# Optimization experiments

Measured on AMD Instinct MI355X. Metric: run time of the kernel, lower is better.

Reference implementation:

```python
import jax, jax.numpy as jnp
import numpy as np

TAU = 2.0
BN_EPS = 1e-5
SG_ALPHA = 4.0
ATTN_SCALE = 0.125
NUM_HEADS = 8
T, B, C, H, W = 2, 16, 256, 64, 64


@jax.custom_vjp
def heaviside(x):
    return (x >= 0.0).astype(x.dtype)

def _hv_fwd(x):
    return (x >= 0.0).astype(x.dtype), x

def _hv_bwd(x, g):
    s = jax.nn.sigmoid(SG_ALPHA * x)
    return (g * SG_ALPHA * s * (1.0 - s),)

heaviside.defvjp(_hv_fwd, _hv_bwd)


def lif(x_seq, v_th):
    # MultiStepLIFNode: v <- v + (x - v)/tau ; spike = H(v - v_th); hard reset to 0 (detached)
    def step(v, x):
        v = v + (x - v) / TAU
        s = heaviside(v - v_th)
        v = v * (1.0 - jax.lax.stop_gradient(s))
        return v, s
    _, spikes = jax.lax.scan(step, jnp.zeros_like(x_seq[0]), x_seq)
    return spikes


def bn1d(x, gamma, beta, mean, var):
    # eval-mode BatchNorm1d over channel axis 2 of [T,B,C,N]
    inv = (gamma / jnp.sqrt(var + BN_EPS)).reshape(1, 1, -1, 1)
    shift = (beta - mean * gamma / jnp.sqrt(var + BN_EPS)).reshape(1, 1, -1, 1)
    return x * inv + shift


def to_heads(t):
    # [T,B,C,N] -> [T,B,h,N,d]
    t_, b_, c_, n_ = t.shape
    d = c_ // NUM_HEADS
    return t.transpose(0, 1, 3, 2).reshape(t_, b_, n_, NUM_HEADS, d).transpose(0, 1, 3, 2, 4)


def setup_inputs() -> dict:
    key = jax.random.key(0)
    ks = jax.random.split(key, 24)
    w_scale = 0.06  # ~1/sqrt(C)
    inp = {
        'x': jax.random.normal(ks[0], (T, B, C, H, W), jnp.float32),
        'wq': jax.random.normal(ks[1], (C, C), jnp.float32) * w_scale,
        'wk': jax.random.normal(ks[2], (C, C), jnp.float32) * w_scale,
        'wv': jax.random.normal(ks[3], (C, C), jnp.float32) * w_scale,
        'wp': jax.random.normal(ks[4], (C, C), jnp.float32) * w_scale,
        'bp': jax.random.normal(ks[5], (C,), jnp.float32) * 0.1,
    }
    i = 6
    for p in ('q', 'k', 'v', 'p'):
        inp[p + '_gamma'] = jax.random.uniform(ks[i], (C,), jnp.float32, 0.5, 1.5); i += 1
        inp[p + '_beta'] = jax.random.normal(ks[i], (C,), jnp.float32) * 0.1; i += 1
        inp[p + '_mean'] = jax.random.normal(ks[i], (C,), jnp.float32) * 0.1; i += 1
        inp[p + '_var'] = jax.random.uniform(ks[i], (C,), jnp.float32, 0.5, 1.5); i += 1
    return inp


def reference(x, wq, wk, wv, wp, bp,
              q_gamma, q_beta, q_mean, q_var,
              k_gamma, k_beta, k_mean, k_var,
              v_gamma, v_beta, v_mean, v_var,
              p_gamma, p_beta, p_mean, p_var):
    t_, b_, c_, h_, w_ = x.shape
    n_ = h_ * w_
    xs = lif(x, 1.0).reshape(t_, b_, c_, n_)  # proj_lif then flatten(3)
    # 1x1 conv == channel matmul, then BN, then LIF (binary spikes)
    q_out = lif(bn1d(jnp.einsum('oc,tbcn->tbon', wq, xs), q_gamma, q_beta, q_mean, q_var), 1.0)
    k_out = lif(bn1d(jnp.einsum('oc,tbcn->tbon', wk, xs), k_gamma, k_beta, k_mean, k_var), 1.0)
    v_out = lif(bn1d(jnp.einsum('oc,tbcn->tbon', wv, xs), v_gamma, v_beta, v_mean, v_var), 1.0)
    q = to_heads(q_out)
    k = to_heads(k_out)
    v = to_heads(v_out)
    # linear attention: (k^T @ v) then q @ (k^T v)
    kv = jnp.einsum('tbhnd,tbhne->tbhde', k, v)  # [T,B,h,d,d]
    attn = jnp.einsum('tbhnd,tbhde->tbhne', q, kv) * ATTN_SCALE
    attn = attn.transpose(0, 1, 2, 4, 3).reshape(t_, b_, c_, n_)
    s = lif(attn, 0.5)  # attn_lif with v_threshold=0.5
    out = jnp.einsum('oc,tbcn->tbon', wp, s) + bp.reshape(1, 1, -1, 1)
    out = bn1d(out, p_gamma, p_beta, p_mean, p_var).reshape(t_, b_, c_, h_, w_)
    return (out, xs, q_out, k_out, v_out)
```

## Files before the change

kernel.cpp:

```cpp
#include <hip/hip_runtime.h>
#include <cstdint>
#include <cstddef>

typedef __attribute__((ext_vector_type(8))) short short8;
typedef __attribute__((ext_vector_type(4))) float floatx4;
typedef __attribute__((ext_vector_type(4))) unsigned int uintx4;
typedef __attribute__((ext_vector_type(4))) unsigned short ushort4x;

#define DEV static __device__ __forceinline__

constexpr int NT = 2, NB = 16, NC = 256, NN = 4096, NHD = 8;
constexpr size_t NE1 = (size_t)NT * NB * NC * NN;
constexpr size_t TSTRIDE = (size_t)NB * NC * NN;

DEV unsigned short f2bf(float x) {
  unsigned int u = __builtin_bit_cast(unsigned int, x);
  unsigned int lsb = (u >> 16) & 1u;
  u += 0x7FFFu + lsb;
  return (unsigned short)(u >> 16);
}
DEV float bfb2f(unsigned short h) {
  unsigned int u = ((unsigned int)h) << 16;
  return __builtin_bit_cast(float, u);
}
DEV unsigned short spike2bf(float s) {
  return (unsigned short)(__builtin_bit_cast(unsigned int, s) >> 16);
}
DEV unsigned int pk2(unsigned short a, unsigned short b) {
  return (unsigned int)a | ((unsigned int)b << 16);
}
typedef __attribute__((address_space(3))) unsigned int lds_u32;
typedef __attribute__((address_space(1))) const unsigned int glb_u32;
DEV void gld_lds16(const void* g, void* l) {
  __builtin_amdgcn_global_load_lds((glb_u32*)g, (lds_u32*)l, 16, 0, 0);
}

__global__ __launch_bounds__(256) void prep_kernel(
    const float* __restrict__ wq, const float* __restrict__ wk, const float* __restrict__ wv,
    const float* __restrict__ wp, const float* __restrict__ bp,
    const float* __restrict__ qg, const float* __restrict__ qb, const float* __restrict__ qm, const float* __restrict__ qva,
    const float* __restrict__ kg, const float* __restrict__ kb, const float* __restrict__ km, const float* __restrict__ kva,
    const float* __restrict__ vg, const float* __restrict__ vb, const float* __restrict__ vm, const float* __restrict__ vva,
    const float* __restrict__ pg, const float* __restrict__ pb, const float* __restrict__ pm, const float* __restrict__ pva,
    unsigned short* __restrict__ Wqkv, unsigned short* __restrict__ Wp,
    float* __restrict__ invqkv, float* __restrict__ shqkv,
    float* __restrict__ invp, float* __restrict__ shp)
{
  int idx = blockIdx.x * 256 + threadIdx.x;
  if (idx < 196608) {
    int o = idx >> 8, c = idx & 255;
    const float* src = (o < 256) ? wq : (o < 512) ? wk : wv;
    float w = src[(size_t)(o & 255) * 256 + c];
    unsigned short h0 = f2bf(w);  float f0 = bfb2f(h0);
    float r1 = w - f0;
    unsigned short h1 = f2bf(r1); float f1 = bfb2f(h1);
    float r2 = r1 - f1;
    unsigned short h2 = f2bf(r2);
    Wqkv[idx] = h0; Wqkv[196608 + idx] = h1; Wqkv[393216 + idx] = h2;
  } else if (idx < 262144) {
    int j = idx - 196608;
    float w = wp[j];
    unsigned short h0 = f2bf(w);  float f0 = bfb2f(h0);
    float r1 = w - f0;
    unsigned short h1 = f2bf(r1); float f1 = bfb2f(h1);
    float r2 = r1 - f1;
    unsigned short h2 = f2bf(r2);
    Wp[j] = h0; Wp[65536 + j] = h1; Wp[131072 + j] = h2;
  } else if (idx < 262912) {
    int i = idx - 262144;
    int p = i >> 8, c = i & 255;
    float g  = (p == 0) ? qg[c] : (p == 1) ? kg[c] : vg[c];
    float be = (p == 0) ? qb[c] : (p == 1) ? kb[c] : vb[c];
    float mn = (p == 0) ? qm[c] : (p == 1) ? km[c] : vm[c];
    float vr = (p == 0) ? qva[c] : (p == 1) ? kva[c] : vva[c];
    float sq = sqrtf(vr + 1e-5f);
    invqkv[i] = g / sq;
    shqkv[i]  = be - (mn * g) / sq;
  } else if (idx < 263168) {
    int c = idx - 262912;
    float sq = sqrtf(pva[c] + 1e-5f);
    float iv = pg[c] / sq;
    invp[c] = iv;
    shp[c]  = pb[c] - (pm[c] * pg[c]) / sq + bp[c] * iv;
  }
}

__global__ __launch_bounds__(256) void lifx_kernel(const float* __restrict__ x,
                                                   float* __restrict__ xs_out,
                                                   unsigned short* __restrict__ xs_t)
{
  __shared__ float tile[2][64][65];
  const int nt = blockIdx.x, ct = blockIdx.y, b = blockIdx.z;
  const int tid = threadIdx.x;
  const int ci = tid >> 2, cq = tid & 3;
  const int n0 = nt * 64, c0 = ct * 64;
  const size_t rowbase = ((size_t)(b * NC + c0 + ci)) * NN + n0 + cq * 16;
  const float* px0 = x + rowbase;
  const float* px1 = x + rowbase + TSTRIDE;
  float* po0 = xs_out + rowbase;
  float* po1 = xs_out + rowbase + TSTRIDE;
  #pragma unroll
  for (int jj = 0; jj < 4; jj++) {
    floatx4 x0 = *(const floatx4*)(px0 + jj * 4);
    floatx4 x1 = *(const floatx4*)(px1 + jj * 4);
    floatx4 s0v, s1v;
    #pragma unroll
    for (int e = 0; e < 4; e++) {
      float v1 = x0[e] * 0.5f;
      float s0 = (v1 >= 1.0f) ? 1.0f : 0.0f;
      float vr = v1 * (1.0f - s0);
      float v2 = vr + (x1[e] - vr) * 0.5f;
      float s1 = (v2 >= 1.0f) ? 1.0f : 0.0f;
      s0v[e] = s0; s1v[e] = s1;
      tile[0][ci][cq * 16 + jj * 4 + e] = s0;
      tile[1][ci][cq * 16 + jj * 4 + e] = s1;
    }
    *(floatx4*)(po0 + jj * 4) = s0v;
    *(floatx4*)(po1 + jj * 4) = s1v;
  }
  __syncthreads();
  const int ni = tid >> 2, cg = tid & 3;
  #pragma unroll
  for (int t = 0; t < 2; t++) {
    unsigned short* dst = xs_t + ((size_t)((t * NB + b) * NN) + n0 + ni) * NC + c0 + cg * 16;
    uintx4 w0, w1;
    #pragma unroll
    for (int p2 = 0; p2 < 4; p2++) {
      w0[p2] = pk2(spike2bf(tile[t][cg * 16 + p2 * 2    ][ni]),
                   spike2bf(tile[t][cg * 16 + p2 * 2 + 1][ni]));
      w1[p2] = pk2(spike2bf(tile[t][cg * 16 + p2 * 2 + 8][ni]),
                   spike2bf(tile[t][cg * 16 + p2 * 2 + 9][ni]));
    }
    *(uintx4*)dst = w0;
    *(uintx4*)(dst + 8) = w1;
  }
}

__global__ __launch_bounds__(256, 3) void qkv_gemm(
    const unsigned short* __restrict__ xs_t,
    const unsigned short* __restrict__ Wsp,
    const float* __restrict__ invv, const float* __restrict__ shv,
    float* __restrict__ dq, float* __restrict__ dk, float* __restrict__ dv)
{
  __shared__ __align__(16) unsigned char smem[33280];
  unsigned short* Al = (unsigned short*)smem;
  unsigned short* Bl = (unsigned short*)(smem + 24576);
  float* yl = (float*)smem;
  const int nt = blockIdx.x, mt = blockIdx.y, b = blockIdx.z;
  const int tid = threadIdx.x;
  const int lane = tid & 63, quad = lane >> 4, l16 = lane & 15;
  const int wave = tid >> 6;
  const int tw = wave >> 1, wm = (wave & 1) * 64;
  floatx4 acc[4][4] = {};

  for (int k0 = 0; k0 < 256; k0 += 32) {
    __syncthreads();
    #pragma unroll
    for (int j = 0; j < 6; j++) {
      int ci = j * 256 + tid;
      int s = ci >> 9, j2 = ci & 511, row = j2 >> 2, kk = j2 & 3;
      const unsigned short* g = Wsp + (size_t)s * 196608 + (size_t)(mt * 128 + row) * 256 + k0 + kk * 8;
      gld_lds16(g, Al + ci * 8);
    }
    #pragma unroll
    for (int j = 0; j < 2; j++) {
      int ci = j * 256 + tid;
      int t = ci >> 8, j2 = ci & 255, row = j2 >> 2, kk = j2 & 3;
      const unsigned short* g = xs_t + ((size_t)((t * NB + b) * NN) + nt * 64 + row) * NC + k0 + kk * 8;
      gld_lds16(g, Bl + ci * 8);
    }
    __syncthreads();

    short8 bfr[4];
    #pragma unroll
    for (int ni = 0; ni < 4; ni++)
      bfr[ni] = *(const short8*)(Bl + ((size_t)(tw * 64 + ni * 16 + l16)) * 32 + quad * 8);
    #pragma unroll
    for (int mi = 0; mi < 4; mi++) {
      const int arow = wm + mi * 16 + l16;
      short8 a0 = *(const short8*)(Al + ((size_t)(          arow)) * 32 + quad * 8);
      short8 a1 = *(const short8*)(Al + ((size_t)(128  +   arow)) * 32 + quad * 8);
      short8 a2 = *(const short8*)(Al + ((size_t)(256  +   arow)) * 32 + quad * 8);
      #pragma unroll
      for (int ni = 0; ni < 4; ni++) {
        acc[mi][ni] = __builtin_amdgcn_mfma_f32_16x16x32_bf16(a0, bfr[ni], acc[mi][ni], 0, 0, 0);
        acc[mi][ni] = __builtin_amdgcn_mfma_f32_16x16x32_bf16(a1, bfr[ni], acc[mi][ni], 0, 0, 0);
        acc[mi][ni] = __builtin_amdgcn_mfma_f32_16x16x32_bf16(a2, bfr[ni], acc[mi][ni], 0, 0, 0);
      }
    }
  }
  __syncthreads();
  if (tw == 0) {
    #pragma unroll
    for (int mi = 0; mi < 4; mi++)
      #pragma unroll
      for (int r = 0; r < 4; r++)
        #pragma unroll
        for (int ni = 0; ni < 4; ni++)
          yl[(size_t)(wm + mi * 16 + quad * 4 + r) * 65 + ni * 16 + l16] = acc[mi][ni][r];
  }
  __syncthreads();
  if (tw == 1) {
    #pragma unroll
    for (int mi = 0; mi < 4; mi++) {
      #pragma unroll
      for (int r = 0; r < 4; r++) {
        const int lrow = wm + mi * 16 + quad * 4 + r;
        const int orow = mt * 128 + lrow;
        const float iv = invv[orow], sh = shv[orow];
        const int widx = orow >> 8, c = orow & 255;
        float* dst = (widx == 0) ? dq : (widx == 1) ? dk : dv;
        #pragma unroll
        for (int ni = 0; ni < 4; ni++) {
          const int n = nt * 64 + ni * 16 + l16;
          float y0 = yl[(size_t)lrow * 65 + ni * 16 + l16] * iv + sh;
          float y1 = acc[mi][ni][r] * iv + sh;
          float v1 = y0 * 0.5f;
          float s0 = (v1 >= 1.0f) ? 1.0f : 0.0f;
          float vr = v1 * (1.0f - s0);
          float v2 = vr + (y1 - vr) * 0.5f;
          float s1 = (v2 >= 1.0f) ? 1.0f : 0.0f;
          dst[(size_t)(b * NC + c) * NN + n] = s0;
          dst[(size_t)((NB + b) * NC + c) * NN + n] = s1;
        }
      }
    }
  }
}

__global__ __launch_bounds__(256) void kv_kernel(const float* __restrict__ kspk,
                                                 const float* __restrict__ vspk,
                                                 float* __restrict__ kvp)
{
  __shared__ __align__(16) unsigned short Kl[32][264];
  __shared__ __align__(16) unsigned short Vl[32][264];
  const int h = blockIdx.x, z = blockIdx.y, ch = blockIdx.z;
  const int tid = threadIdx.x;
  const int wave = tid >> 6, lane = tid & 63, quad = lane >> 4, l16 = lane & 15;
  const int dh = wave & 1, eh = wave >> 1;
  const size_t base = (size_t)z * NC * NN + (size_t)h * 32 * NN + (size_t)ch * 1024;
  floatx4 acc = {0.f, 0.f, 0.f, 0.f};
  for (int n0 = 0; n0 < 1024; n0 += 256) {
    __syncthreads();
    for (int i = tid; i < 2048; i += 256) {
      int row = i >> 6, c4 = (i & 63) * 4;
      const size_t g = base + (size_t)row * NN + n0 + c4;
      floatx4 kk = *(const floatx4*)(kspk + g);
      floatx4 vv = *(const floatx4*)(vspk + g);
      ushort4x ks, vs;
      #pragma unroll
      for (int e = 0; e < 4; e++) { ks[e] = spike2bf(kk[e]); vs[e] = spike2bf(vv[e]); }
      *(ushort4x*)&Kl[row][c4] = ks;
      *(ushort4x*)&Vl[row][c4] = vs;
    }
    __syncthreads();
    #pragma unroll
    for (int i = 0; i < 8; i++) {
      short8 ka = *(const short8*)&Kl[dh * 16 + l16][i * 32 + quad * 8];
      short8 vb = *(const short8*)&Vl[eh * 16 + l16][i * 32 + quad * 8];
      acc = __builtin_amdgcn_mfma_f32_16x16x32_bf16(ka, vb, acc, 0, 0, 0);
    }
  }
  float* o = kvp + ((size_t)((ch * 32 + z) * NHD + h)) * 1024;
  #pragma unroll
  for (int r = 0; r < 4; r++)
    o[(dh * 16 + quad * 4 + r) * 32 + eh * 16 + l16] = acc[r];
}

__global__ __launch_bounds__(256) void attn_kernel(const float* __restrict__ qspk,
                                                   const float* __restrict__ kvp,
                                                   unsigned short* __restrict__ s_t)
{
  __shared__ float kvl[2][32][33];
  __shared__ __align__(8) float ql[32][258];
  const int nb = blockIdx.x, h = blockIdx.y, b = blockIdx.z;
  const int tid = threadIdx.x;
  const int wave = tid >> 6, lane = tid & 63, quad = lane >> 4, l16 = lane & 15;
  for (int i = tid; i < 2048; i += 256) {
    int t = i >> 10, j = i & 1023;
    size_t o = ((size_t)((t * NB + b) * NHD + h) << 10) + j;
    float v = kvp[o] + kvp[o + 262144] + kvp[o + 524288] + kvp[o + 786432];
    kvl[t][j >> 5][j & 31] = v;
  }
  __syncthreads();
  short8 bf[2][2][2];
  #pragma unroll
  for (int t = 0; t < 2; t++) {
    #pragma unroll
    for (int eh = 0; eh < 2; eh++) {
      short8 bh, bl;
      #pragma unroll
      for (int j = 0; j < 8; j++) {
        float v = kvl[t][quad * 8 + j][eh * 16 + l16];
        unsigned short h0 = f2bf(v);
        float lo = v - bfb2f(h0);
        bh[j] = (short)h0;
        bl[j] = (short)f2bf(lo);
      }
      bf[t][0][eh] = bh; bf[t][1][eh] = bl;
    }
  }
  floatx4 acc[2][4][2] = {};
  #pragma unroll
  for (int t = 0; t < 2; t++) {
    __syncthreads();
    const float* qp = qspk + ((size_t)((t * NB + b) * NC + h * 32)) * NN + nb * 256;
    for (int i = tid; i < 4096; i += 256) {
      int row = i >> 7, c2 = (i & 127) * 2;
      *(float2*)&ql[row][c2] = *(const float2*)(qp + (size_t)row * NN + c2);
    }
    __syncthreads();
    #pragma unroll
    for (int nt = 0; nt < 4; nt++) {
      const int nrow = wave * 64 + nt * 16 + l16;
      short8 af;
      #pragma unroll
      for (int j = 0; j < 8; j++)
        af[j] = (short)spike2bf(ql[quad * 8 + j][nrow]);
      #pragma unroll
      for (int eh = 0; eh < 2; eh++) {
        acc[t][nt][eh] = __builtin_amdgcn_mfma_f32_16x16x32_bf16(af, bf[t][0][eh], acc[t][nt][eh], 0, 0, 0);
        acc[t][nt][eh] = __builtin_amdgcn_mfma_f32_16x16x32_bf16(af, bf[t][1][eh], acc[t][nt][eh], 0, 0, 0);
      }
    }
  }
  const int n0 = nb * 256 + wave * 64;
  #pragma unroll
  for (int nt = 0; nt < 4; nt++) {
    #pragma unroll
    for (int r = 0; r < 4; r++) {
      const int n = n0 + nt * 16 + quad * 4 + r;
      unsigned short* d0 = s_t + ((size_t)(b * NN) + n) * NC + h * 32 + l16;
      unsigned short* d1 = s_t + ((size_t)((NB + b) * NN) + n) * NC + h * 32 + l16;
      #pragma unroll
      for (int eh = 0; eh < 2; eh++) {
        float a0 = acc[0][nt][eh][r] * 0.125f;
        float a1 = acc[1][nt][eh][r] * 0.125f;
        float v1 = a0 * 0.5f;
        float s0 = (v1 >= 0.5f) ? 1.f : 0.f;
        float vr = v1 * (1.f - s0);
        float v2 = vr + (a1 - vr) * 0.5f;
        float s1 = (v2 >= 0.5f) ? 1.f : 0.f;
        d0[eh * 16] = s0 != 0.f ? (unsigned short)0x3F80 : (unsigned short)0;
        d1[eh * 16] = s1 != 0.f ? (unsigned short)0x3F80 : (unsigned short)0;
      }
    }
  }
}

__global__ __launch_bounds__(256, 3) void p_gemm(
    const unsigned short* __restrict__ s_t,
    const unsigned short* __restrict__ Wsp,
    const float* __restrict__ invv, const float* __restrict__ shv,
    float* __restrict__ dout)
{
  __shared__ __align__(16) unsigned char smem[32768];
  unsigned short* Al = (unsigned short*)smem;
  unsigned short* Bl = (unsigned short*)(smem + 24576);
  const int nt = blockIdx.x, mt = blockIdx.y, z = blockIdx.z;
  const int tid = threadIdx.x;
  const int lane = tid & 63, quad = lane >> 4, l16 = lane & 15;
  const int wave = tid >> 6;
  const int wm = (wave & 1) * 64, wn = (wave >> 1) * 64;
  floatx4 acc[4][4] = {};

  for (int k0 = 0; k0 < 256; k0 += 32) {
    __syncthreads();
    #pragma unroll
    for (int j = 0; j < 6; j++) {
      int ci = j * 256 + tid;
      int s = ci >> 9, j2 = ci & 511, row = j2 >> 2, kk = j2 & 3;
      const unsigned short* g = Wsp + (size_t)s * 65536 + (size_t)(mt * 128 + row) * 256 + k0 + kk * 8;
      gld_lds16(g, Al + ci * 8);
    }
    #pragma unroll
    for (int j = 0; j < 2; j++) {
      int ci = j * 256 + tid;
      int row = ci >> 2, kk = ci & 3;
      const unsigned short* g = s_t + ((size_t)(z * NN) + nt * 128 + row) * NC + k0 + kk * 8;
      gld_lds16(g, Bl + ci * 8);
    }
    __syncthreads();

    short8 bfr[4];
    #pragma unroll
    for (int ni = 0; ni < 4; ni++)
      bfr[ni] = *(const short8*)(Bl + ((size_t)(wn + ni * 16 + l16)) * 32 + quad * 8);
    #pragma unroll
    for (int mi = 0; mi < 4; mi++) {
      const int arow = wm + mi * 16 + l16;
      short8 a0 = *(const short8*)(Al + ((size_t)(        arow)) * 32 + quad * 8);
      short8 a1 = *(const short8*)(Al + ((size_t)(128 +   arow)) * 32 + quad * 8);
      short8 a2 = *(const short8*)(Al + ((size_t)(256 +   arow)) * 32 + quad * 8);
      #pragma unroll
      for (int ni = 0; ni < 4; ni++) {
        acc[mi][ni] = __builtin_amdgcn_mfma_f32_16x16x32_bf16(a0, bfr[ni], acc[mi][ni], 0, 0, 0);
        acc[mi][ni] = __builtin_amdgcn_mfma_f32_16x16x32_bf16(a1, bfr[ni], acc[mi][ni], 0, 0, 0);
        acc[mi][ni] = __builtin_amdgcn_mfma_f32_16x16x32_bf16(a2, bfr[ni], acc[mi][ni], 0, 0, 0);
      }
    }
  }
  #pragma unroll
  for (int mi = 0; mi < 4; mi++) {
    #pragma unroll
    for (int r = 0; r < 4; r++) {
      const int orow = mt * 128 + wm + mi * 16 + quad * 4 + r;
      const float iv = invv[orow], sh = shv[orow];
      #pragma unroll
      for (int ni = 0; ni < 4; ni++) {
        const int n = nt * 128 + wn + ni * 16 + l16;
        dout[((size_t)(z * NC + orow)) * NN + n] = acc[mi][ni][r] * iv + sh;
      }
    }
  }
}

extern "C" void kernel_launch(void* const* d_in, const int* in_sizes, int n_in,
                              void* d_out, int out_size, void* d_ws, size_t ws_size,
                              hipStream_t stream) {
  (void)in_sizes; (void)n_in; (void)out_size; (void)ws_size;
  const float* x  = (const float*)d_in[0];
  const float* wq = (const float*)d_in[1];
  const float* wk = (const float*)d_in[2];
  const float* wv = (const float*)d_in[3];
  const float* wp = (const float*)d_in[4];
  const float* bp = (const float*)d_in[5];
  const float* qg = (const float*)d_in[6],  *qb = (const float*)d_in[7];
  const float* qm = (const float*)d_in[8],  *qva = (const float*)d_in[9];
  const float* kg = (const float*)d_in[10], *kb = (const float*)d_in[11];
  const float* km = (const float*)d_in[12], *kva = (const float*)d_in[13];
  const float* vg = (const float*)d_in[14], *vb = (const float*)d_in[15];
  const float* vm = (const float*)d_in[16], *vva = (const float*)d_in[17];
  const float* pg = (const float*)d_in[18], *pb = (const float*)d_in[19];
  const float* pm = (const float*)d_in[20], *pva = (const float*)d_in[21];

  float* out = (float*)d_out;
  float* xs  = out + NE1;
  float* dq  = out + 2 * NE1;
  float* dk  = out + 3 * NE1;
  float* dv  = out + 4 * NE1;

  char* ws = (char*)d_ws;
  unsigned short* xs_t = (unsigned short*)ws;
  unsigned short* s_t  = (unsigned short*)ws;
  unsigned short* Wqkv = (unsigned short*)(ws + 67108864);
  unsigned short* Wp   = (unsigned short*)(ws + 68288512);
  float* kvp           = (float*)(ws + 68681728);
  float* invqkv        = (float*)(ws + 72876032);
  float* shqkv         = invqkv + 768;
  float* invp          = shqkv + 768;
  float* shp           = invp + 256;

  prep_kernel<<<1028, 256, 0, stream>>>(wq, wk, wv, wp, bp,
                                        qg, qb, qm, qva, kg, kb, km, kva,
                                        vg, vb, vm, vva, pg, pb, pm, pva,
                                        Wqkv, Wp, invqkv, shqkv, invp, shp);
  lifx_kernel<<<dim3(64, 4, 16), 256, 0, stream>>>(x, xs, xs_t);
  qkv_gemm<<<dim3(64, 6, 16), 256, 0, stream>>>(xs_t, Wqkv, invqkv, shqkv, dq, dk, dv);
  kv_kernel<<<dim3(8, 32, 4), 256, 0, stream>>>(dk, dv, kvp);
  attn_kernel<<<dim3(16, 8, 16), 256, 0, stream>>>(dq, kvp, s_t);
  p_gemm<<<dim3(32, 2, 32), 256, 0, stream>>>(s_t, Wp, invp, shp, out);
}
```

Measured before the change: 1.093 ms.

## Pack binary spikes into bitmasks and compute KV via popcount, swizzle LDS

```diff
diff --git a/kernel.cpp b/kernel.cpp
--- a/kernel.cpp
+++ b/kernel.cpp
@@ -29,6 +29,7 @@
 DEV unsigned int pk2(unsigned short a, unsigned short b) {
   return (unsigned int)a | ((unsigned int)b << 16);
 }
+DEV int swz(int fr, int kk) { return fr * 4 + (kk ^ ((fr >> 1) & 3)); }
 typedef __attribute__((address_space(3))) unsigned int lds_u32;
 typedef __attribute__((address_space(1))) const unsigned int glb_u32;
 DEV void gld_lds16(const void* g, void* l) {
@@ -140,7 +141,9 @@
     const unsigned short* __restrict__ xs_t,
     const unsigned short* __restrict__ Wsp,
     const float* __restrict__ invv, const float* __restrict__ shv,
-    float* __restrict__ dq, float* __restrict__ dk, float* __restrict__ dv)
+    float* __restrict__ dq, float* __restrict__ dk, float* __restrict__ dv,
+    unsigned short* __restrict__ qbits, unsigned short* __restrict__ kbits,
+    unsigned short* __restrict__ vbits)
 {
   __shared__ __align__(16) unsigned char smem[33280];
   unsigned short* Al = (unsigned short*)smem;
@@ -158,29 +161,35 @@
     #pragma unroll
     for (int j = 0; j < 6; j++) {
       int ci = j * 256 + tid;
-      int s = ci >> 9, j2 = ci & 511, row = j2 >> 2, kk = j2 & 3;
+      int fr = ci >> 2;
+      int kk = (ci & 3) ^ ((fr >> 1) & 3);
+      int s = fr >> 7, row = fr & 127;
       const unsigned short* g = Wsp + (size_t)s * 196608 + (size_t)(mt * 128 + row) * 256 + k0 + kk * 8;
-      gld_lds16(g, Al + ci * 8);
+      gld_lds16(g, Al + (size_t)ci * 8);
     }
     #pragma unroll
     for (int j = 0; j < 2; j++) {
       int ci = j * 256 + tid;
-      int t = ci >> 8, j2 = ci & 255, row = j2 >> 2, kk = j2 & 3;
+      int fr = ci >> 2;
+      int kk = (ci & 3) ^ ((fr >> 1) & 3);
+      int t = fr >> 6, row = fr & 63;
       const unsigned short* g = xs_t + ((size_t)((t * NB + b) * NN) + nt * 64 + row) * NC + k0 + kk * 8;
-      gld_lds16(g, Bl + ci * 8);
+      gld_lds16(g, Bl + (size_t)ci * 8);
     }
     __syncthreads();
 
     short8 bfr[4];
     #pragma unroll
-    for (int ni = 0; ni < 4; ni++)
-      bfr[ni] = *(const short8*)(Bl + ((size_t)(tw * 64 + ni * 16 + l16)) * 32 + quad * 8);
+    for (int ni = 0; ni < 4; ni++) {
+      int fr = tw * 64 + ni * 16 + l16;
+      bfr[ni] = *(const short8*)(Bl + (size_t)swz(fr, quad) * 8);
+    }
     #pragma unroll
     for (int mi = 0; mi < 4; mi++) {
-      const int arow = wm + mi * 16 + l16;
-      short8 a0 = *(const short8*)(Al + ((size_t)(          arow)) * 32 + quad * 8);
-      short8 a1 = *(const short8*)(Al + ((size_t)(128  +   arow)) * 32 + quad * 8);
-      short8 a2 = *(const short8*)(Al + ((size_t)(256  +   arow)) * 32 + quad * 8);
+      const int r0 = wm + mi * 16 + l16;
+      short8 a0 = *(const short8*)(Al + (size_t)swz(      r0, quad) * 8);
+      short8 a1 = *(const short8*)(Al + (size_t)swz(128 + r0, quad) * 8);
+      short8 a2 = *(const short8*)(Al + (size_t)swz(256 + r0, quad) * 8);
       #pragma unroll
       for (int ni = 0; ni < 4; ni++) {
         acc[mi][ni] = __builtin_amdgcn_mfma_f32_16x16x32_bf16(a0, bfr[ni], acc[mi][ni], 0, 0, 0);
@@ -210,6 +219,7 @@
         const float iv = invv[orow], sh = shv[orow];
         const int widx = orow >> 8, c = orow & 255;
         float* dst = (widx == 0) ? dq : (widx == 1) ? dk : dv;
+        unsigned short* bb = (widx == 0) ? qbits : (widx == 1) ? kbits : vbits;
         #pragma unroll
         for (int ni = 0; ni < 4; ni++) {
           const int n = nt * 64 + ni * 16 + l16;
@@ -222,65 +232,66 @@
           float s1 = (v2 >= 1.0f) ? 1.0f : 0.0f;
           dst[(size_t)(b * NC + c) * NN + n] = s0;
           dst[(size_t)((NB + b) * NC + c) * NN + n] = s1;
+          unsigned long long bl0 = __ballot(s0 != 0.0f);
+          unsigned long long bl1 = __ballot(s1 != 0.0f);
+          if (l16 == 0) {
+            const int w16 = nt * 4 + ni;
+            bb[(size_t)b        * 65536 + (size_t)c * 256 + w16] = (unsigned short)(bl0 >> (quad * 16));
+            bb[(size_t)(NB + b) * 65536 + (size_t)c * 256 + w16] = (unsigned short)(bl1 >> (quad * 16));
+          }
         }
       }
     }
   }
 }
 
-__global__ __launch_bounds__(256) void kv_kernel(const float* __restrict__ kspk,
-                                                 const float* __restrict__ vspk,
-                                                 float* __restrict__ kvp)
-{
-  __shared__ __align__(16) unsigned short Kl[32][264];
-  __shared__ __align__(16) unsigned short Vl[32][264];
-  const int h = blockIdx.x, z = blockIdx.y, ch = blockIdx.z;
+__global__ __launch_bounds__(256) void kv_kernel(const unsigned long long* __restrict__ kb,
+                                                 const unsigned long long* __restrict__ vb,
+                                                 float* __restrict__ kvout)
+{
+  __shared__ unsigned long long Kl[32 * 65];
+  __shared__ unsigned long long Vl[32 * 65];
+  const int h = blockIdx.x, z = blockIdx.y;
   const int tid = threadIdx.x;
-  const int wave = tid >> 6, lane = tid & 63, quad = lane >> 4, l16 = lane & 15;
-  const int dh = wave & 1, eh = wave >> 1;
-  const size_t base = (size_t)z * NC * NN + (size_t)h * 32 * NN + (size_t)ch * 1024;
-  floatx4 acc = {0.f, 0.f, 0.f, 0.f};
-  for (int n0 = 0; n0 < 1024; n0 += 256) {
-    __syncthreads();
-    for (int i = tid; i < 2048; i += 256) {
-      int row = i >> 6, c4 = (i & 63) * 4;
-      const size_t g = base + (size_t)row * NN + n0 + c4;
-      floatx4 kk = *(const floatx4*)(kspk + g);
-      floatx4 vv = *(const floatx4*)(vspk + g);
-      ushort4x ks, vs;
-      #pragma unroll
-      for (int e = 0; e < 4; e++) { ks[e] = spike2bf(kk[e]); vs[e] = spike2bf(vv[e]); }
-      *(ushort4x*)&Kl[row][c4] = ks;
-      *(ushort4x*)&Vl[row][c4] = vs;
-    }
-    __syncthreads();
-    #pragma unroll
-    for (int i = 0; i < 8; i++) {
-      short8 ka = *(const short8*)&Kl[dh * 16 + l16][i * 32 + quad * 8];
-      short8 vb = *(const short8*)&Vl[eh * 16 + l16][i * 32 + quad * 8];
-      acc = __builtin_amdgcn_mfma_f32_16x16x32_bf16(ka, vb, acc, 0, 0, 0);
-    }
-  }
-  float* o = kvp + ((size_t)((ch * 32 + z) * NHD + h)) * 1024;
-  #pragma unroll
-  for (int r = 0; r < 4; r++)
-    o[(dh * 16 + quad * 4 + r) * 32 + eh * 16 + l16] = acc[r];
-}
-
-__global__ __launch_bounds__(256) void attn_kernel(const float* __restrict__ qspk,
-                                                   const float* __restrict__ kvp,
-                                                   unsigned short* __restrict__ s_t)
+  for (int i = tid; i < 2048; i += 256) {
+    int row = i >> 6, w = i & 63;
+    size_t g = (size_t)z * 16384 + (size_t)(h * 32 + row) * 64 + w;
+    Kl[row * 65 + w] = kb[g];
+    Vl[row * 65 + w] = vb[g];
+  }
+  __syncthreads();
+  const int d = tid & 31, e0 = tid >> 5;
+  int acc0 = 0, acc1 = 0, acc2 = 0, acc3 = 0;
+  for (int w = 0; w < 64; w++) {
+    unsigned long long ku = Kl[d * 65 + w];
+    acc0 += __popcll(ku & Vl[(e0     ) * 65 + w]);
+    acc1 += __popcll(ku & Vl[(e0 +  8) * 65 + w]);
+    acc2 += __popcll(ku & Vl[(e0 + 16) * 65 + w]);
+    acc3 += __popcll(ku & Vl[(e0 + 24) * 65 + w]);
+  }
+  float* o = kvout + ((size_t)(z * NHD + h) << 10);
+  o[d * 32 + e0     ] = (float)acc0;
+  o[d * 32 + e0 +  8] = (float)acc1;
+  o[d * 32 + e0 + 16] = (float)acc2;
+  o[d * 32 + e0 + 24] = (float)acc3;
+}
+
+__global__ __launch_bounds__(256) void attn_kernel(const unsigned short* __restrict__ qb16,
+                                                   const float* __restrict__ kvout,
+                                                   unsigned short* __restrict__ sb16)
 {
   __shared__ float kvl[2][32][33];
-  __shared__ __align__(8) float ql[32][258];
+  __shared__ unsigned short qt[2][32][16];
   const int nb = blockIdx.x, h = blockIdx.y, b = blockIdx.z;
   const int tid = threadIdx.x;
   const int wave = tid >> 6, lane = tid & 63, quad = lane >> 4, l16 = lane & 15;
   for (int i = tid; i < 2048; i += 256) {
     int t = i >> 10, j = i & 1023;
-    size_t o = ((size_t)((t * NB + b) * NHD + h) << 10) + j;
-    float v = kvp[o] + kvp[o + 262144] + kvp[o + 524288] + kvp[o + 786432];
-    kvl[t][j >> 5][j & 31] = v;
+    kvl[t][j >> 5][j & 31] = kvout[((size_t)((t * NB + b) * NHD + h) << 10) + j];
+  }
+  for (int i = tid; i < 1024; i += 256) {
+    int t = i >> 9, j = i & 511, row = j >> 4, w = j & 15;
+    qt[t][row][w] = qb16[(size_t)(t * NB + b) * 65536 + (size_t)(h * 32 + row) * 256 + nb * 16 + w];
   }
   __syncthreads();
   short8 bf[2][2][2];
@@ -303,20 +314,15 @@
   floatx4 acc[2][4][2] = {};
   #pragma unroll
   for (int t = 0; t < 2; t++) {
-    __syncthreads();
-    const float* qp = qspk + ((size_t)((t * NB + b) * NC + h * 32)) * NN + nb * 256;
-    for (int i = tid; i < 4096; i += 256) {
-      int row = i >> 7, c2 = (i & 127) * 2;
-      *(float2*)&ql[row][c2] = *(const float2*)(qp + (size_t)row * NN + c2);
-    }
-    __syncthreads();
     #pragma unroll
     for (int nt = 0; nt < 4; nt++) {
-      const int nrow = wave * 64 + nt * 16 + l16;
+      const int wv = wave * 4 + nt;
       short8 af;
       #pragma unroll
-      for (int j = 0; j < 8; j++)
-        af[j] = (short)spike2bf(ql[quad * 8 + j][nrow]);
+      for (int j = 0; j < 8; j++) {
+        unsigned short w = qt[t][quad * 8 + j][wv];
+        af[j] = (short)(((w >> l16) & 1) ? 0x3F80 : 0);
+      }
       #pragma unroll
       for (int eh = 0; eh < 2; eh++) {
         acc[t][nt][eh] = __builtin_amdgcn_mfma_f32_16x16x32_bf16(af, bf[t][0][eh], acc[t][nt][eh], 0, 0, 0);
@@ -330,8 +336,6 @@
     #pragma unroll
     for (int r = 0; r < 4; r++) {
       const int n = n0 + nt * 16 + quad * 4 + r;
-      unsigned short* d0 = s_t + ((size_t)(b * NN) + n) * NC + h * 32 + l16;
-      unsigned short* d1 = s_t + ((size_t)((NB + b) * NN) + n) * NC + h * 32 + l16;
       #pragma unroll
       for (int eh = 0; eh < 2; eh++) {
         float a0 = acc[0][nt][eh][r] * 0.125f;
@@ -341,15 +345,20 @@
         float vr = v1 * (1.f - s0);
         float v2 = vr + (a1 - vr) * 0.5f;
         float s1 = (v2 >= 0.5f) ? 1.f : 0.f;
-        d0[eh * 16] = s0 != 0.f ? (unsigned short)0x3F80 : (unsigned short)0;
-        d1[eh * 16] = s1 != 0.f ? (unsigned short)0x3F80 : (unsigned short)0;
+        unsigned long long bl0 = __ballot(s0 != 0.f);
+        unsigned long long bl1 = __ballot(s1 != 0.f);
+        if (l16 == 0) {
+          const int w16 = h * 2 + eh;
+          sb16[(size_t)b        * 65536 + (size_t)n * 16 + w16] = (unsigned short)(bl0 >> (quad * 16));
+          sb16[(size_t)(NB + b) * 65536 + (size_t)n * 16 + w16] = (unsigned short)(bl1 >> (quad * 16));
+        }
       }
     }
   }
 }
 
 __global__ __launch_bounds__(256, 3) void p_gemm(
-    const unsigned short* __restrict__ s_t,
+    const unsigned short* __restrict__ sb16,
     const unsigned short* __restrict__ Wsp,
     const float* __restrict__ invv, const float* __restrict__ shv,
     float* __restrict__ dout)
@@ -363,35 +372,44 @@
   const int wave = tid >> 6;
   const int wm = (wave & 1) * 64, wn = (wave >> 1) * 64;
   floatx4 acc[4][4] = {};
+  const int brow = tid & 127, bhalf = tid >> 7;
 
   for (int k0 = 0; k0 < 256; k0 += 32) {
     __syncthreads();
     #pragma unroll
     for (int j = 0; j < 6; j++) {
       int ci = j * 256 + tid;
-      int s = ci >> 9, j2 = ci & 511, row = j2 >> 2, kk = j2 & 3;
+      int fr = ci >> 2;
+      int kk = (ci & 3) ^ ((fr >> 1) & 3);
+      int s = fr >> 7, row = fr & 127;
       const unsigned short* g = Wsp + (size_t)s * 65536 + (size_t)(mt * 128 + row) * 256 + k0 + kk * 8;
-      gld_lds16(g, Al + ci * 8);
-    }
-    #pragma unroll
-    for (int j = 0; j < 2; j++) {
-      int ci = j * 256 + tid;
-      int row = ci >> 2, kk = ci & 3;
-      const unsigned short* g = s_t + ((size_t)(z * NN) + nt * 128 + row) * NC + k0 + kk * 8;
-      gld_lds16(g, Bl + ci * 8);
+      gld_lds16(g, Al + (size_t)ci * 8);
+    }
+    {
+      unsigned short wb = sb16[(size_t)z * 65536 + (size_t)(nt * 128 + brow) * 16 + (k0 >> 4) + bhalf];
+      uintx4 lo4, hi4;
+      #pragma unroll
+      for (int p = 0; p < 4; p++) {
+        lo4[p] = pk2(((wb >> (2 * p)) & 1) ? 0x3F80 : 0, ((wb >> (2 * p + 1)) & 1) ? 0x3F80 : 0);
+        hi4[p] = pk2(((wb >> (8 + 2 * p)) & 1) ? 0x3F80 : 0, ((wb >> (9 + 2 * p)) & 1) ? 0x3F80 : 0);
+      }
+      *(uintx4*)(Bl + (size_t)swz(brow, bhalf * 2)     * 8) = lo4;
+      *(uintx4*)(Bl + (size_t)swz(brow, bhalf * 2 + 1) * 8) = hi4;
     }
     __syncthreads();
 
     short8 bfr[4];
     #pragma unroll
-    for (int ni = 0; ni < 4; ni++)
-      bfr[ni] = *(const short8*)(Bl + ((size_t)(wn + ni * 16 + l16)) * 32 + quad * 8);
+    for (int ni = 0; ni < 4; ni++) {
+      int fr = wn + ni * 16 + l16;
+      bfr[ni] = *(const short8*)(Bl + (size_t)swz(fr, quad) * 8);
+    }
     #pragma unroll
     for (int mi = 0; mi < 4; mi++) {
-      const int arow = wm + mi * 16 + l16;
-      short8 a0 = *(const short8*)(Al + ((size_t)(        arow)) * 32 + quad * 8);
-      short8 a1 = *(const short8*)(Al + ((size_t)(128 +   arow)) * 32 + quad * 8);
-      short8 a2 = *(const short8*)(Al + ((size_t)(256 +   arow)) * 32 + quad * 8);
+      const int r0 = wm + mi * 16 + l16;
+      short8 a0 = *(const short8*)(Al + (size_t)swz(      r0, quad) * 8);
+      short8 a1 = *(const short8*)(Al + (size_t)swz(128 + r0, quad) * 8);
+      short8 a2 = *(const short8*)(Al + (size_t)swz(256 + r0, quad) * 8);
       #pragma unroll
       for (int ni = 0; ni < 4; ni++) {
         acc[mi][ni] = __builtin_amdgcn_mfma_f32_16x16x32_bf16(a0, bfr[ni], acc[mi][ni], 0, 0, 0);
@@ -441,23 +459,28 @@
   float* dv  = out + 4 * NE1;
 
   char* ws = (char*)d_ws;
-  unsigned short* xs_t = (unsigned short*)ws;
-  unsigned short* s_t  = (unsigned short*)ws;
-  unsigned short* Wqkv = (unsigned short*)(ws + 67108864);
-  unsigned short* Wp   = (unsigned short*)(ws + 68288512);
-  float* kvp           = (float*)(ws + 68681728);
-  float* invqkv        = (float*)(ws + 72876032);
-  float* shqkv         = invqkv + 768;
-  float* invp          = shqkv + 768;
-  float* shp           = invp + 256;
+  unsigned short* xs_t  = (unsigned short*)ws;
+  unsigned short* Wqkv  = (unsigned short*)(ws + 67108864);
+  unsigned short* Wp    = (unsigned short*)(ws + 68288512);
+  float* kvout          = (float*)(ws + 68681728);
+  unsigned short* qbits = (unsigned short*)(ws + 69730304);
+  unsigned short* kbits = (unsigned short*)(ws + 73924608);
+  unsigned short* vbits = (unsigned short*)(ws + 78118912);
+  unsigned short* sbits = (unsigned short*)(ws + 82313216);
+  float* invqkv         = (float*)(ws + 86507520);
+  float* shqkv          = invqkv + 768;
+  float* invp           = shqkv + 768;
+  float* shp            = invp + 256;
 
   prep_kernel<<<1028, 256, 0, stream>>>(wq, wk, wv, wp, bp,
                                         qg, qb, qm, qva, kg, kb, km, kva,
                                         vg, vb, vm, vva, pg, pb, pm, pva,
                                         Wqkv, Wp, invqkv, shqkv, invp, shp);
   lifx_kernel<<<dim3(64, 4, 16), 256, 0, stream>>>(x, xs, xs_t);
-  qkv_gemm<<<dim3(64, 6, 16), 256, 0, stream>>>(xs_t, Wqkv, invqkv, shqkv, dq, dk, dv);
-  kv_kernel<<<dim3(8, 32, 4), 256, 0, stream>>>(dk, dv, kvp);
-  attn_kernel<<<dim3(16, 8, 16), 256, 0, stream>>>(dq, kvp, s_t);
-  p_gemm<<<dim3(32, 2, 32), 256, 0, stream>>>(s_t, Wp, invp, shp, out);
-}
+  qkv_gemm<<<dim3(64, 6, 16), 256, 0, stream>>>(xs_t, Wqkv, invqkv, shqkv,
+                                                dq, dk, dv, qbits, kbits, vbits);
+  kv_kernel<<<dim3(8, 32), 256, 0, stream>>>((const unsigned long long*)kbits,
+                                             (const unsigned long long*)vbits, kvout);
+  attn_kernel<<<dim3(16, 8, 16), 256, 0, stream>>>(qbits, kvout, sbits);
+  p_gemm<<<dim3(32, 2, 32), 256, 0, stream>>>(sbits, Wp, invp, shp, out);
+}
```

New measurement: 1.035 ms. 1.06x faster.
